# Kernel tuning notes

Measured on AMD Instinct MI355X. Metric: run time of the kernel, lower is better.

## Reference

```python
import jax, jax.numpy as jnp
from jax import lax
import numpy as np

B, N, D = 32, 8192, 256
EPS = 1e-06        # module eps
NUM = 1e-06        # numerator epsilon in tan_theta
BN_EPS = 1e-05     # torch BatchNorm1d default
SLOPE = 0.2        # LeakyReLU negative_slope

REG = jnp.array([[-1, -1, -1, 0, 0, 0, 1, 1, 1],
                 [-1,  0,  1, -1, 0, 1, -1, 0, 1]], dtype=jnp.float32)  # [2,9]


def conv1d(x, w, b):
    # x: [B,C,N], w: [O,C,3], pad=1 -> [B,O,N]
    y = lax.conv_general_dilated(x, w, (1,), [(1, 1)],
                                 dimension_numbers=('NCH', 'OIH', 'NCH'))
    return y + b[None, :, None]


def batchnorm(x, gamma, beta):
    # training-mode BatchNorm1d over (B, N) per channel, biased variance
    m = x.mean(axis=(0, 2), keepdims=True)
    v = ((x - m) ** 2).mean(axis=(0, 2), keepdims=True)
    return gamma[None, :, None] * (x - m) * lax.rsqrt(v + BN_EPS) + beta[None, :, None]


def setup_inputs() -> dict:
    key = jax.random.key(0)
    ks = jax.random.split(key, 12)
    s = 0.05
    return {
        'pts':      jax.random.normal(ks[0], (B, 2, N), jnp.float32),
        'feats':    jax.random.normal(ks[1], (B, D, N), jnp.float32),
        'rot_w':    jax.random.normal(ks[2], (4, D, 3), jnp.float32) * s,
        'rot_b':    jax.random.normal(ks[3], (4,), jnp.float32) * s,
        'trans_w':  jax.random.normal(ks[4], (2, D, 3), jnp.float32) * s,
        'trans_b':  jax.random.normal(ks[5], (2,), jnp.float32) * s,
        'pos_w':    jax.random.normal(ks[6], (2, 20, 3), jnp.float32) * s,
        'pos_b':    jax.random.normal(ks[7], (2,), jnp.float32) * s,
        'pos_g':    jnp.ones((2,), jnp.float32),
        'pos_beta': jnp.zeros((2,), jnp.float32),
        'ori_w':    jax.random.normal(ks[8], (2, 2, 3), jnp.float32) * s,
        'ori_b':    jax.random.normal(ks[9], (2,), jnp.float32) * s,
        'ori_g':    jnp.ones((2,), jnp.float32),
        'ori_beta': jnp.zeros((2,), jnp.float32),
    }


def compute_offset(feats, rot_w, rot_b, trans_w, trans_b):
    b, _, n = feats.shape
    tm = conv1d(feats, rot_w, rot_b)                       # [B,4,N]
    tm = tm.transpose(0, 2, 1).reshape(b, n, 2, 2)         # per-point 2x2
    transformed = jnp.einsum('bnij,jk->bnik', tm, REG)     # [B,N,2,9]
    offset = transformed - REG                             # broadcast [2,9]
    # transpose(1,2).reshape(B,N,18).permute -> interleaved (x0,y0,x1,y1,...)
    offset = offset.transpose(0, 1, 3, 2).reshape(b, n, 18).transpose(0, 2, 1)  # [B,18,N]
    translation = conv1d(feats, trans_w, trans_b)          # [B,2,N]
    # even channels += tx, odd channels += ty
    off = offset.reshape(b, 9, 2, n) + translation[:, None, :, :]
    return off.reshape(b, 18, n)


def reference(pts, feats, rot_w, rot_b, trans_w, trans_b,
              pos_w, pos_b, pos_g, pos_beta,
              ori_w, ori_b, ori_g, ori_beta):
    b, _, n = pts.shape
    offset = compute_offset(feats, rot_w, rot_b, trans_w, trans_b)  # [B,18,N]

    # geo_position branch
    x = jnp.concatenate([pts, offset], axis=1)             # [B,20,N]
    x = conv1d(x, pos_w, pos_b)                            # [B,2,N]
    x = batchnorm(x, pos_g, pos_beta)
    x = jnp.where(x >= 0, x, SLOPE * x)                    # LeakyReLU(0.2)

    # geo_orientation branch
    off_x = offset[:, 0::2, :]                             # [B,9,N]
    off_y = offset[:, 1::2, :]
    rad = jnp.arctan((off_y + NUM) / (off_x + EPS))        # [B,9,N]
    main_rad = rad.max(axis=1)                             # [B,N]
    c, s = jnp.cos(main_rad), jnp.sin(main_rad)
    # rotation[b,n] = [[cos, sin], [-sin, cos]]
    rot = jnp.stack([jnp.stack([c, s], -1), jnp.stack([-s, c], -1)], -2)  # [B,N,2,2]
    x = jnp.einsum('bxn,bnxy->byn', x, rot)                # rotate 2-d coords
    x = conv1d(x, ori_w, ori_b)
    x = batchnorm(x, ori_g, ori_beta)
    return x
```

## Files before the change

kernel.cpp:

```cpp
#include <hip/hip_runtime.h>
#include <math.h>

#define NPTS 8192
#define DCH  256
#define BB   32
#define TOTPT (BB * NPTS)

#define X1_OFF    0
#define COS_OFF   (X1_OFF + BB * 2 * NPTS)
#define SIN_OFF   (COS_OFF + TOTPT)
#define X5_OFF    (SIN_OFF + TOTPT)
#define STATS_OFF (X5_OFF + BB * 2 * NPTS)

__device__ __forceinline__ void block_reduce_atomic4(float v0, float v1,
                                                     float v2, float v3,
                                                     float* dst)
{
#pragma unroll
    for (int off = 32; off > 0; off >>= 1) {
        v0 += __shfl_down(v0, off, 64);
        v1 += __shfl_down(v1, off, 64);
        v2 += __shfl_down(v2, off, 64);
        v3 += __shfl_down(v3, off, 64);
    }
    __shared__ float red[4][4];
    const int wave = threadIdx.x >> 6, lane = threadIdx.x & 63;
    if (lane == 0) {
        red[wave][0] = v0; red[wave][1] = v1; red[wave][2] = v2; red[wave][3] = v3;
    }
    __syncthreads();
    if (threadIdx.x == 0) {
        float a0 = 0, a1 = 0, a2 = 0, a3 = 0;
#pragma unroll
        for (int w = 0; w < 4; ++w) {
            a0 += red[w][0]; a1 += red[w][1]; a2 += red[w][2]; a3 += red[w][3];
        }
        atomicAdd(dst + 0, a0); atomicAdd(dst + 1, a1);
        atomicAdd(dst + 2, a2); atomicAdd(dst + 3, a3);
    }
}

__global__ __launch_bounds__(256) void kernAB(
    const float* __restrict__ pts, const float* __restrict__ feats,
    const float* __restrict__ rot_w, const float* __restrict__ rot_b,
    const float* __restrict__ trans_w, const float* __restrict__ trans_b,
    const float* __restrict__ pos_w, const float* __restrict__ pos_b,
    float* __restrict__ x1, float* __restrict__ cosA, float* __restrict__ sinA,
    float* __restrict__ stats)
{
    const int blk  = blockIdx.x;
    const int b    = blk >> 5;
    const int n0   = (blk & 31) << 8;
    const int tid  = threadIdx.x;
    const int wave = tid >> 6;
    const int lane = tid & 63;
    const int p    = n0 + (lane << 2);

    const float* fb = feats + (size_t)b * DCH * NPTS;

    __shared__ float red[3][64][25];
    __shared__ float hw4[4][12];
    __shared__ float Tsh[6][260];

    float acc[6][4];
#pragma unroll
    for (int o = 0; o < 6; ++o)
#pragma unroll
        for (int j = 0; j < 4; ++j) acc[o][j] = 0.0f;

    const int c0 = __builtin_amdgcn_readfirstlane(wave << 6);

    const float lmask = (p > 0) ? 1.0f : 0.0f;
    const int   lidx  = (p > 0) ? (p - 1) : 0;
    const float rmask = (p + 4 < NPTS) ? 1.0f : 0.0f;
    const int   ridx  = (p + 4 < NPTS) ? (p + 4) : 0;

    const float* fr = fb + (size_t)c0 * NPTS;

#pragma unroll 4
    for (int cc = 0; cc < 64; ++cc) {
        const int c = c0 + cc;
        const float4 v = *(const float4*)(fr + p);
        const float fl = fr[lidx] * lmask;
        const float fd = fr[ridx] * rmask;
        const float f[6] = { fl, v.x, v.y, v.z, v.w, fd };
#pragma unroll
        for (int o = 0; o < 6; ++o) {
            const float* wp = (o < 4) ? (rot_w + ((size_t)o * DCH + c) * 3)
                                      : (trans_w + ((size_t)(o - 4) * DCH + c) * 3);
            const float w0 = wp[0], w1 = wp[1], w2 = wp[2];
#pragma unroll
            for (int j = 0; j < 4; ++j)
                acc[o][j] += w0 * f[j] + w1 * f[j + 1] + w2 * f[j + 2];
        }
        fr += NPTS;
    }

    float hh[12];
    {
        const float* fc = fb + (size_t)tid * NPTS;
        const int iA = (n0 >= 2) ? (n0 - 2) : 0;
        const int iB = (n0 >= 1) ? (n0 - 1) : 0;
        const float a0 = fc[iA], a1 = fc[iB], a2 = fc[n0];
        const int jB = (n0 + 256 <= NPTS - 1) ? (n0 + 256) : (NPTS - 1);
        const int jC = (n0 + 257 <= NPTS - 1) ? (n0 + 257) : (NPTS - 1);
        const float b0 = fc[n0 + 255], b1 = fc[jB], b2 = fc[jC];
#pragma unroll
        for (int o = 0; o < 6; ++o) {
            const float* wp = (o < 4) ? (rot_w + ((size_t)o * DCH + tid) * 3)
                                      : (trans_w + ((size_t)(o - 4) * DCH + tid) * 3);
            const float w0 = wp[0], w1 = wp[1], w2 = wp[2];
            hh[o]     = w0 * a0 + w1 * a1 + w2 * a2;
            hh[6 + o] = w0 * b0 + w1 * b1 + w2 * b2;
        }
    }
#pragma unroll
    for (int off = 32; off > 0; off >>= 1)
#pragma unroll
        for (int j = 0; j < 12; ++j)
            hh[j] += __shfl_down(hh[j], off, 64);

    if (wave >= 1) {
#pragma unroll
        for (int o = 0; o < 6; ++o)
#pragma unroll
            for (int j = 0; j < 4; ++j)
                red[wave - 1][lane][o * 4 + j] = acc[o][j];
    }
    if (lane == 0) {
#pragma unroll
        for (int j = 0; j < 12; ++j) hw4[wave][j] = hh[j];
    }
    __syncthreads();

    if (wave == 0) {
#pragma unroll
        for (int q = 0; q < 3; ++q)
#pragma unroll
            for (int o = 0; o < 6; ++o)
#pragma unroll
                for (int j = 0; j < 4; ++j)
                    acc[o][j] += red[q][lane][o * 4 + j];
#pragma unroll
        for (int o = 0; o < 6; ++o) {
            const float bias = (o < 4) ? rot_b[o] : trans_b[o - 4];
#pragma unroll
            for (int j = 0; j < 4; ++j)
                Tsh[o][1 + (lane << 2) + j] = acc[o][j] + bias;
        }
    }
    if (tid < 12) {
        const int o = tid % 6, side = tid / 6;
        float v = hw4[0][tid] + hw4[1][tid] + hw4[2][tid] + hw4[3][tid];
        v += (o < 4) ? rot_b[o] : trans_b[o - 4];
        Tsh[o][side ? 257 : 0] = v;
    }
    __syncthreads();

    const int n = n0 + tid;
    float tm[6][3];
#pragma unroll
    for (int o = 0; o < 6; ++o)
#pragma unroll
        for (int k = 0; k < 3; ++k)
            tm[o][k] = Tsh[o][tid + k];

    float xs0 = pos_b[0], xs1 = pos_b[1];
    float mz = -INFINITY;

#pragma unroll
    for (int m3 = 0; m3 < 3; ++m3) {
        const int m   = n + m3 - 1;
        const float msk = (m >= 0 && m < NPTS) ? 1.0f : 0.0f;
        const int mc  = (m < 0) ? 0 : ((m >= NPTS) ? NPTS - 1 : m);

        const float pa = pts[((size_t)b * 2 + 0) * NPTS + mc];
        const float pb = pts[((size_t)b * 2 + 1) * NPTS + mc];

        const float o0 = tm[0][m3] - 1.0f, o1 = tm[1][m3];
        const float o2 = tm[2][m3],        o3 = tm[3][m3] - 1.0f;
        const float tr0 = tm[4][m3],       tr1 = tm[5][m3];

        float p0 = pos_w[0 * 60 + 0 * 3 + m3] * pa + pos_w[0 * 60 + 1 * 3 + m3] * pb;
        float p1 = pos_w[1 * 60 + 0 * 3 + m3] * pa + pos_w[1 * 60 + 1 * 3 + m3] * pb;
#pragma unroll
        for (int k = 0; k < 9; ++k) {
            const float R0 = (float)(k / 3 - 1);
            const float R1 = (float)(k % 3 - 1);
            const float cx = o0 * R0 + o1 * R1 + tr0;
            const float cy = o2 * R0 + o3 * R1 + tr1;
            p0 += pos_w[0 * 60 + (2 + 2 * k) * 3 + m3] * cx
                + pos_w[0 * 60 + (3 + 2 * k) * 3 + m3] * cy;
            p1 += pos_w[1 * 60 + (2 + 2 * k) * 3 + m3] * cx
                + pos_w[1 * 60 + (3 + 2 * k) * 3 + m3] * cy;
            if (m3 == 1) {
                const float z = (cy + 1e-6f) / (cx + 1e-6f);
                mz = fmaxf(mz, z);
            }
        }
        xs0 += msk * p0;
        xs1 += msk * p1;
    }

    const float mr = atanf(mz);
    float sv, cv;
    sincosf(mr, &sv, &cv);

    const int g = (b << 13) + n;
    x1[((size_t)b * 2 + 0) * NPTS + n] = xs0;
    x1[((size_t)b * 2 + 1) * NPTS + n] = xs1;
    cosA[g] = cv;
    sinA[g] = sv;

    block_reduce_atomic4(xs0, xs1, xs0 * xs0, xs1 * xs1,
                         stats + ((blk & 15) << 2));
}

__global__ __launch_bounds__(256) void kernD(
    const float* __restrict__ x1,
    const float* __restrict__ cosA, const float* __restrict__ sinA,
    const float* __restrict__ pos_g, const float* __restrict__ pos_beta,
    const float* __restrict__ ori_w, const float* __restrict__ ori_b,
    float* __restrict__ stats, float* __restrict__ x5)
{
    const int gg = blockIdx.x * 256 + threadIdx.x;
    const int b = gg >> 13;
    const int n = gg & (NPTS - 1);

    float s0 = 0, s1 = 0, s2 = 0, s3 = 0;
#pragma unroll
    for (int q = 0; q < 16; ++q) {
        s0 += stats[q * 4 + 0]; s1 += stats[q * 4 + 1];
        s2 += stats[q * 4 + 2]; s3 += stats[q * 4 + 3];
    }
    const float cntInv = 1.0f / (float)TOTPT;
    const float m0 = s0 * cntInv, m1 = s1 * cntInv;
    const float var0 = s2 * cntInv - m0 * m0;
    const float var1 = s3 * cntInv - m1 * m1;
    const float i0 = rsqrtf(var0 + 1e-5f), i1 = rsqrtf(var1 + 1e-5f);
    const float g0 = pos_g[0], g1 = pos_g[1];
    const float be0 = pos_beta[0], be1 = pos_beta[1];

    float x4a[3], x4b[3];
#pragma unroll
    for (int m3 = 0; m3 < 3; ++m3) {
        const int m   = n + m3 - 1;
        const float msk = (m >= 0 && m < NPTS) ? 1.0f : 0.0f;
        const int mc  = (m < 0) ? 0 : ((m >= NPTS) ? NPTS - 1 : m);
        float y0 = x1[((size_t)b * 2 + 0) * NPTS + mc];
        float y1 = x1[((size_t)b * 2 + 1) * NPTS + mc];
        y0 = g0 * (y0 - m0) * i0 + be0;
        y1 = g1 * (y1 - m1) * i1 + be1;
        y0 = (y0 >= 0.0f) ? y0 : 0.2f * y0;
        y1 = (y1 >= 0.0f) ? y1 : 0.2f * y1;
        const float cv = cosA[(b << 13) + mc];
        const float sv = sinA[(b << 13) + mc];
        x4a[m3] = (y0 * cv - y1 * sv) * msk;
        x4b[m3] = (y0 * sv + y1 * cv) * msk;
    }

    float z0 = ori_b[0], z1 = ori_b[1];
#pragma unroll
    for (int k = 0; k < 3; ++k) {
        z0 += ori_w[0 * 6 + 0 * 3 + k] * x4a[k] + ori_w[0 * 6 + 1 * 3 + k] * x4b[k];
        z1 += ori_w[1 * 6 + 0 * 3 + k] * x4a[k] + ori_w[1 * 6 + 1 * 3 + k] * x4b[k];
    }
    x5[((size_t)b * 2 + 0) * NPTS + n] = z0;
    x5[((size_t)b * 2 + 1) * NPTS + n] = z1;

    block_reduce_atomic4(z0, z1, z0 * z0, z1 * z1,
                         stats + 64 + ((blockIdx.x & 15) << 2));
}

__global__ __launch_bounds__(256) void kernE(
    const float* __restrict__ x5, const float* __restrict__ stats,
    const float* __restrict__ ori_g, const float* __restrict__ ori_beta,
    float* __restrict__ out)
{
    const int gg = blockIdx.x * 256 + threadIdx.x;
    const int o = (gg >> 13) & 1;
    float sm = 0, sq = 0;
#pragma unroll
    for (int q = 0; q < 16; ++q) {
        sm += stats[64 + q * 4 + o];
        sq += stats[64 + q * 4 + 2 + o];
    }
    const float cntInv = 1.0f / (float)TOTPT;
    const float m  = sm * cntInv;
    const float vv = sq * cntInv - m * m;
    const float inv = rsqrtf(vv + 1e-5f);
    out[gg] = ori_g[o] * (x5[gg] - m) * inv + ori_beta[o];
}

extern "C" void kernel_launch(void* const* d_in, const int* in_sizes, int n_in,
                              void* d_out, int out_size, void* d_ws, size_t ws_size,
                              hipStream_t stream)
{
    const float* pts      = (const float*)d_in[0];
    const float* feats    = (const float*)d_in[1];
    const float* rot_w    = (const float*)d_in[2];
    const float* rot_b    = (const float*)d_in[3];
    const float* trans_w  = (const float*)d_in[4];
    const float* trans_b  = (const float*)d_in[5];
    const float* pos_w    = (const float*)d_in[6];
    const float* pos_b    = (const float*)d_in[7];
    const float* pos_g    = (const float*)d_in[8];
    const float* pos_beta = (const float*)d_in[9];
    const float* ori_w    = (const float*)d_in[10];
    const float* ori_b    = (const float*)d_in[11];
    const float* ori_g    = (const float*)d_in[12];
    const float* ori_beta = (const float*)d_in[13];

    float* ws    = (float*)d_ws;
    float* x1    = ws + X1_OFF;
    float* cosA  = ws + COS_OFF;
    float* sinA  = ws + SIN_OFF;
    float* x5    = ws + X5_OFF;
    float* stats = ws + STATS_OFF;

    hipMemsetAsync(stats, 0, 128 * sizeof(float), stream);

    kernAB<<<1024, 256, 0, stream>>>(pts, feats, rot_w, rot_b, trans_w, trans_b,
                                     pos_w, pos_b, x1, cosA, sinA, stats);
    kernD<<<1024, 256, 0, stream>>>(x1, cosA, sinA, pos_g, pos_beta,
                                    ori_w, ori_b, stats, x5);
    kernE<<<2048, 256, 0, stream>>>(x5, stats, ori_g, ori_beta, (float*)d_out);
}
```

Measured before the change: 499.2 us.

## Split fused conv/geometry kernel and parallelize conv over channel groups with atomics

Splits the fused kernel into a channel-split convolution kernel (4096 blocks, each covering 64 channels for a 256-point tile) that atomically accumulates the 6 conv outputs into a global buffer, followed by a per-point geometry kernel that reads the buffer with the neighbor halo. The aim is more parallelism and occupancy while streaming the 256 MB feature tensor, and it drops the halo recomputation. In exchange it adds a memset and atomic traffic on a 6 MB intermediate plus an extra kernel launch and a global round trip.

```diff
diff --git a/kernel.cpp b/kernel.cpp
--- a/kernel.cpp
+++ b/kernel.cpp
@@ -6,7 +6,8 @@
 #define BB   32
 #define TOTPT (BB * NPTS)
 
-#define X1_OFF    0
+#define T_OFF     0
+#define X1_OFF    (T_OFF + BB * 6 * NPTS)
 #define COS_OFF   (X1_OFF + BB * 2 * NPTS)
 #define SIN_OFF   (COS_OFF + TOTPT)
 #define X5_OFF    (SIN_OFF + TOTPT)
@@ -40,35 +41,30 @@
     }
 }
 
-__global__ __launch_bounds__(256) void kernAB(
-    const float* __restrict__ pts, const float* __restrict__ feats,
-    const float* __restrict__ rot_w, const float* __restrict__ rot_b,
-    const float* __restrict__ trans_w, const float* __restrict__ trans_b,
-    const float* __restrict__ pos_w, const float* __restrict__ pos_b,
-    float* __restrict__ x1, float* __restrict__ cosA, float* __restrict__ sinA,
-    float* __restrict__ stats)
+__global__ __launch_bounds__(256) void convA(
+    const float* __restrict__ feats,
+    const float* __restrict__ rot_w,
+    const float* __restrict__ trans_w,
+    float* __restrict__ T)
 {
     const int blk  = blockIdx.x;
-    const int b    = blk >> 5;
-    const int n0   = (blk & 31) << 8;
-    const int tid  = threadIdx.x;
-    const int wave = tid >> 6;
-    const int lane = tid & 63;
+    const int cg   = blk & 3;
+    const int tile = (blk >> 2) & 31;
+    const int b    = blk >> 7;
+    const int n0   = tile << 8;
+    const int wave = threadIdx.x >> 6;
+    const int lane = threadIdx.x & 63;
     const int p    = n0 + (lane << 2);
 
     const float* fb = feats + (size_t)b * DCH * NPTS;
 
-    __shared__ float red[3][64][25];
-    __shared__ float hw4[4][12];
-    __shared__ float Tsh[6][260];
-
     float acc[6][4];
 #pragma unroll
     for (int o = 0; o < 6; ++o)
 #pragma unroll
         for (int j = 0; j < 4; ++j) acc[o][j] = 0.0f;
 
-    const int c0 = __builtin_amdgcn_readfirstlane(wave << 6);
+    const int c0 = __builtin_amdgcn_readfirstlane((cg << 6) + (wave << 4));
 
     const float lmask = (p > 0) ? 1.0f : 0.0f;
     const int   lidx  = (p > 0) ? (p - 1) : 0;
@@ -77,8 +73,8 @@
 
     const float* fr = fb + (size_t)c0 * NPTS;
 
-#pragma unroll 4
-    for (int cc = 0; cc < 64; ++cc) {
+#pragma unroll 8
+    for (int cc = 0; cc < 16; ++cc) {
         const int c = c0 + cc;
         const float4 v = *(const float4*)(fr + p);
         const float fl = fr[lidx] * lmask;
@@ -96,30 +92,7 @@
         fr += NPTS;
     }
 
-    float hh[12];
-    {
-        const float* fc = fb + (size_t)tid * NPTS;
-        const int iA = (n0 >= 2) ? (n0 - 2) : 0;
-        const int iB = (n0 >= 1) ? (n0 - 1) : 0;
-        const float a0 = fc[iA], a1 = fc[iB], a2 = fc[n0];
-        const int jB = (n0 + 256 <= NPTS - 1) ? (n0 + 256) : (NPTS - 1);
-        const int jC = (n0 + 257 <= NPTS - 1) ? (n0 + 257) : (NPTS - 1);
-        const float b0 = fc[n0 + 255], b1 = fc[jB], b2 = fc[jC];
-#pragma unroll
-        for (int o = 0; o < 6; ++o) {
-            const float* wp = (o < 4) ? (rot_w + ((size_t)o * DCH + tid) * 3)
-                                      : (trans_w + ((size_t)(o - 4) * DCH + tid) * 3);
-            const float w0 = wp[0], w1 = wp[1], w2 = wp[2];
-            hh[o]     = w0 * a0 + w1 * a1 + w2 * a2;
-            hh[6 + o] = w0 * b0 + w1 * b1 + w2 * b2;
-        }
-    }
-#pragma unroll
-    for (int off = 32; off > 0; off >>= 1)
-#pragma unroll
-        for (int j = 0; j < 12; ++j)
-            hh[j] += __shfl_down(hh[j], off, 64);
-
+    __shared__ float red[3][64][25];
     if (wave >= 1) {
 #pragma unroll
         for (int o = 0; o < 6; ++o)
@@ -127,12 +100,7 @@
             for (int j = 0; j < 4; ++j)
                 red[wave - 1][lane][o * 4 + j] = acc[o][j];
     }
-    if (lane == 0) {
-#pragma unroll
-        for (int j = 0; j < 12; ++j) hw4[wave][j] = hh[j];
-    }
     __syncthreads();
-
     if (wave == 0) {
 #pragma unroll
         for (int q = 0; q < 3; ++q)
@@ -143,27 +111,29 @@
                     acc[o][j] += red[q][lane][o * 4 + j];
 #pragma unroll
         for (int o = 0; o < 6; ++o) {
-            const float bias = (o < 4) ? rot_b[o] : trans_b[o - 4];
+            float* dst = T + ((size_t)b * 6 + o) * NPTS + p;
 #pragma unroll
             for (int j = 0; j < 4; ++j)
-                Tsh[o][1 + (lane << 2) + j] = acc[o][j] + bias;
+                atomicAdd(dst + j, acc[o][j]);
         }
     }
-    if (tid < 12) {
-        const int o = tid % 6, side = tid / 6;
-        float v = hw4[0][tid] + hw4[1][tid] + hw4[2][tid] + hw4[3][tid];
-        v += (o < 4) ? rot_b[o] : trans_b[o - 4];
-        Tsh[o][side ? 257 : 0] = v;
-    }
-    __syncthreads();
-
-    const int n = n0 + tid;
-    float tm[6][3];
-#pragma unroll
-    for (int o = 0; o < 6; ++o)
-#pragma unroll
-        for (int k = 0; k < 3; ++k)
-            tm[o][k] = Tsh[o][tid + k];
+}
+
+__global__ __launch_bounds__(256) void kernB(
+    const float* __restrict__ pts, const float* __restrict__ T,
+    const float* __restrict__ rot_b, const float* __restrict__ trans_b,
+    const float* __restrict__ pos_w, const float* __restrict__ pos_b,
+    float* __restrict__ x1, float* __restrict__ cosA, float* __restrict__ sinA,
+    float* __restrict__ stats)
+{
+    const int g = blockIdx.x * 256 + threadIdx.x;
+    const int b = g >> 13;
+    const int n = g & (NPTS - 1);
+
+    float rb[6];
+#pragma unroll
+    for (int o = 0; o < 4; ++o) rb[o] = rot_b[o];
+    rb[4] = trans_b[0]; rb[5] = trans_b[1];
 
     float xs0 = pos_b[0], xs1 = pos_b[1];
     float mz = -INFINITY;
@@ -174,12 +144,17 @@
         const float msk = (m >= 0 && m < NPTS) ? 1.0f : 0.0f;
         const int mc  = (m < 0) ? 0 : ((m >= NPTS) ? NPTS - 1 : m);
 
+        float t[6];
+#pragma unroll
+        for (int o = 0; o < 6; ++o)
+            t[o] = T[((size_t)b * 6 + o) * NPTS + mc] + rb[o];
+
         const float pa = pts[((size_t)b * 2 + 0) * NPTS + mc];
         const float pb = pts[((size_t)b * 2 + 1) * NPTS + mc];
 
-        const float o0 = tm[0][m3] - 1.0f, o1 = tm[1][m3];
-        const float o2 = tm[2][m3],        o3 = tm[3][m3] - 1.0f;
-        const float tr0 = tm[4][m3],       tr1 = tm[5][m3];
+        const float o0 = t[0] - 1.0f, o1 = t[1];
+        const float o2 = t[2],        o3 = t[3] - 1.0f;
+        const float tr0 = t[4],       tr1 = t[5];
 
         float p0 = pos_w[0 * 60 + 0 * 3 + m3] * pa + pos_w[0 * 60 + 1 * 3 + m3] * pb;
         float p1 = pos_w[1 * 60 + 0 * 3 + m3] * pa + pos_w[1 * 60 + 1 * 3 + m3] * pb;
@@ -206,14 +181,13 @@
     float sv, cv;
     sincosf(mr, &sv, &cv);
 
-    const int g = (b << 13) + n;
     x1[((size_t)b * 2 + 0) * NPTS + n] = xs0;
     x1[((size_t)b * 2 + 1) * NPTS + n] = xs1;
     cosA[g] = cv;
     sinA[g] = sv;
 
     block_reduce_atomic4(xs0, xs1, xs0 * xs0, xs1 * xs1,
-                         stats + ((blk & 15) << 2));
+                         stats + ((blockIdx.x & 15) << 2));
 }
 
 __global__ __launch_bounds__(256) void kernD(
@@ -312,16 +286,19 @@
     const float* ori_beta = (const float*)d_in[13];
 
     float* ws    = (float*)d_ws;
+    float* T     = ws + T_OFF;
     float* x1    = ws + X1_OFF;
     float* cosA  = ws + COS_OFF;
     float* sinA  = ws + SIN_OFF;
     float* x5    = ws + X5_OFF;
     float* stats = ws + STATS_OFF;
 
+    hipMemsetAsync(T, 0, (size_t)BB * 6 * NPTS * sizeof(float), stream);
     hipMemsetAsync(stats, 0, 128 * sizeof(float), stream);
 
-    kernAB<<<1024, 256, 0, stream>>>(pts, feats, rot_w, rot_b, trans_w, trans_b,
-                                     pos_w, pos_b, x1, cosA, sinA, stats);
+    convA<<<4096, 256, 0, stream>>>(feats, rot_w, trans_w, T);
+    kernB<<<1024, 256, 0, stream>>>(pts, T, rot_b, trans_b, pos_w, pos_b,
+                                    x1, cosA, sinA, stats);
     kernD<<<1024, 256, 0, stream>>>(x1, cosA, sinA, pos_g, pos_beta,
                                     ori_w, ori_b, stats, x5);
     kernE<<<2048, 256, 0, stream>>>(x5, stats, ori_g, ori_beta, (float*)d_out);
```

New measurement: 536.7 us. 7.5% more time.
